# Kernel tuning notes

Hardware: AMD Instinct MI355X
Metric: run time of the kernel (lower is better)

## Reference

```python
import jax, jax.numpy as jnp
import numpy as np

B, H, S, D = 4, 8, 4096, 64

def setup_inputs() -> dict:
    key = jax.random.key(0)
    kq, kk, kv = jax.random.split(key, 3)
    Q = jax.random.normal(kq, (B, H, S, D), dtype=jnp.float32)
    K = jax.random.normal(kk, (B, H, S, D), dtype=jnp.float32)
    V = jax.random.normal(kv, (B, H, S, D), dtype=jnp.float32)
    return {"Q": Q, "K": K, "V": V}

def reference(Q, K, V):
    scale = 1.0 / jnp.sqrt(jnp.float32(Q.shape[-1]))
    # scores: [B, H, S, S]
    scores = jnp.einsum('bhqd,bhkd->bhqk', Q, K) * scale
    attn = jax.nn.softmax(scores, axis=-1)
    # out: [B, H, S, D]
    return jnp.einsum('bhqk,bhkd->bhqd', attn, V)
```

## Files before the change

kernel.cpp:

```cpp
#include <hip/hip_runtime.h>
#include <hip/hip_bf16.h>

typedef float  f32x16 __attribute__((ext_vector_type(16)));
typedef __bf16 bf16x8 __attribute__((ext_vector_type(8)));
typedef __bf16 bf16x4 __attribute__((ext_vector_type(4)));
typedef __bf16 bf16x2 __attribute__((ext_vector_type(2)));
typedef int    i32x2v __attribute__((ext_vector_type(2)));
typedef int    i32x4v __attribute__((ext_vector_type(4)));

#define SEQ   4096
#define DDIM  64
#define KB    64
#define NT    (SEQ / KB)
#define TILEB 16384
#define WSNEED (32ull * NT * TILEB)
#define SCL   0.18033688011112042f
#define DEFT  16.0f

#if __has_builtin(__builtin_amdgcn_exp2f)
#define EXP2(x) __builtin_amdgcn_exp2f(x)
#else
#define EXP2(x) __expf((x) * 0.6931471805599453f)
#endif

__device__ __forceinline__ int swzb(int row) {
  return (row & 7) ^ ((row >> 3) & 3);
}

__device__ __forceinline__ void pswap32(int &x, int &y) {
#if __has_builtin(__builtin_amdgcn_permlane32_swap)
  i32x2v r = __builtin_amdgcn_permlane32_swap(x, y, false, false);
  x = r[0]; y = r[1];
#else
  asm volatile("v_permlane32_swap_b32 %0, %1" : "+v"(x), "+v"(y));
#endif
}

__device__ __forceinline__ bf16x8 mkfrag(int a, int b, int c, int d) {
  i32x4v v; v[0] = a; v[1] = b; v[2] = c; v[3] = d;
  return __builtin_bit_cast(bf16x8, v);
}

__device__ __forceinline__ float max8(const f32x16& s, int o) {
  float m = fmaxf(fmaxf(s[o+0], s[o+1]), s[o+2]);
  m = fmaxf(fmaxf(m, s[o+3]), s[o+4]);
  m = fmaxf(fmaxf(m, s[o+5]), s[o+6]);
  return fmaxf(m, s[o+7]);
}

__global__ __launch_bounds__(256)
void prep(const float* __restrict__ Kg, const float* __restrict__ Vg,
          char* __restrict__ KVb)
{
  int i = blockIdx.x * 256 + threadIdx.x;
  if (i < (1 << 20)) {
    int row = i >> 3, s_in = i & 7;
    int bh = row >> 12, r = row & 4095, t = r >> 6, kv = r & 63;
    const float* src = Kg + (size_t)row * 64 + s_in * 8;
    float4 f0 = *(const float4*)(src);
    float4 f1 = *(const float4*)(src + 4);
    bf16x8 p;
    p[0] = (__bf16)f0.x; p[1] = (__bf16)f0.y; p[2] = (__bf16)f0.z; p[3] = (__bf16)f0.w;
    p[4] = (__bf16)f1.x; p[5] = (__bf16)f1.y; p[6] = (__bf16)f1.z; p[7] = (__bf16)f1.w;
    char* dst = KVb + (size_t)(bh * NT + t) * TILEB + kv * 128 + ((s_in ^ swzb(kv)) * 16);
    *(bf16x8*)dst = p;
  } else {
    int j = i - (1 << 20);
    int d = j & 63, rest = j >> 6;
    int kvg = rest & 7, t = (rest >> 3) & 63, bh = rest >> 9;
    const float* src = Vg + (size_t)bh * (SEQ * DDIM) + (t * 64 + kvg * 8) * 64 + d;
    bf16x8 p;
    #pragma unroll
    for (int jj = 0; jj < 8; ++jj) p[jj] = (__bf16)src[jj * 64];
    char* dst = KVb + (size_t)(bh * NT + t) * TILEB + 8192 + d * 128
              + ((kvg ^ swzb(d)) * 16);
    *(bf16x8*)dst = p;
  }
}

__global__ __launch_bounds__(256, 4)
void fattn(const float* __restrict__ Qg, const char* __restrict__ KVb,
           float* __restrict__ Og)
{
  __shared__ __align__(16) char smem[2 * TILEB];

  const int tid  = threadIdx.x;
  const int w    = tid >> 6;
  const int lane = tid & 63;
  const int q31  = lane & 31;
  const int h    = lane >> 5;

  int wg = (int)blockIdx.x;
  wg = (wg & 7) * 128 + (wg >> 3);
  const int bh = wg >> 5;
  const int qb = wg & 31;
  const size_t base = (size_t)bh * (SEQ * DDIM);
  const int qrow = qb * 128 + w * 32 + q31;

  bf16x8 aq[4];
  {
    const float* qp = Qg + base + (size_t)qrow * DDIM + 8 * h;
    #pragma unroll
    for (int c = 0; c < 4; ++c) {
      float4 f0 = *(const float4*)(qp + 16 * c);
      float4 f1 = *(const float4*)(qp + 16 * c + 4);
      aq[c][0] = (__bf16)(f0.x * SCL);
      aq[c][1] = (__bf16)(f0.y * SCL);
      aq[c][2] = (__bf16)(f0.z * SCL);
      aq[c][3] = (__bf16)(f0.w * SCL);
      aq[c][4] = (__bf16)(f1.x * SCL);
      aq[c][5] = (__bf16)(f1.y * SCL);
      aq[c][6] = (__bf16)(f1.z * SCL);
      aq[c][7] = (__bf16)(f1.w * SCL);
    }
  }

  const char* kvt = KVb + (size_t)bh * (NT * TILEB);
  const int soff = tid * 16;

  const int swr = swzb(q31) << 4;
  int kaddr[4];
  #pragma unroll
  for (int c = 0; c < 4; ++c)
    kaddr[c] = q31 * 128 + ((32 * c + 16 * h) ^ swr);

  f32x16 o0 = {}, o1 = {};
  float mrow = 0.f, lsum = 0.f;
  int pk[2][8];

  auto softmax_pack = [&](f32x16& s0, f32x16& s1) {
    float m0 = max8(s0, 0), m1 = max8(s0, 8);
    float m2 = max8(s1, 0), m3 = max8(s1, 8);
    float pm = fmaxf(fmaxf(m0, m1), fmaxf(m2, m3));
    if (!__all(pm <= mrow + DEFT)) {
      float tm = fmaxf(pm, __shfl_xor(pm, 32));
      float mn = fmaxf(mrow, tm);
      float corr = EXP2(mrow - mn);
      o0 *= corr; o1 *= corr; lsum *= corr;
      mrow = mn;
    }
    #pragma unroll
    for (int r = 0; r < 16; ++r) s0[r] = EXP2(s0[r] - mrow);
    #pragma unroll
    for (int r = 0; r < 16; ++r) s1[r] = EXP2(s1[r] - mrow);
    f32x16 ts = s0 + s1;
    lsum += ((((ts[0]+ts[1])+(ts[2]+ts[3])) + ((ts[4]+ts[5])+(ts[6]+ts[7])))
          +  (((ts[8]+ts[9])+(ts[10]+ts[11])) + ((ts[12]+ts[13])+(ts[14]+ts[15]))));
    #pragma unroll
    for (int u = 0; u < 8; ++u) {
      bf16x2 p0; p0[0] = (__bf16)s0[2*u]; p0[1] = (__bf16)s0[2*u+1];
      pk[0][u] = __builtin_bit_cast(int, p0);
      bf16x2 p1; p1[0] = (__bf16)s1[2*u]; p1[1] = (__bf16)s1[2*u+1];
      pk[1][u] = __builtin_bit_cast(int, p1);
    }
    #pragma unroll
    for (int m = 0; m < 2; ++m) {
      pswap32(pk[m][0], pk[m][2]);
      pswap32(pk[m][1], pk[m][3]);
      pswap32(pk[m][4], pk[m][6]);
      pswap32(pk[m][5], pk[m][7]);
    }
  };

  {
    const char* sp = kvt + soff;
    #pragma unroll
    for (int c = 0; c < 4; ++c)
      *(bf16x8*)(smem + soff + c * 4096) = *(const bf16x8*)(sp + c * 4096);
  }
  __syncthreads();

  for (int t = 0; t < NT; ++t) {
    const int cur  = (t & 1) << 14;
    const int nxtb = cur ^ TILEB;
    const bool more = (t + 1) < NT;

    bf16x8 st0, st1, st2, st3;
    if (more) {
      const char* sp = kvt + (size_t)(t + 1) * TILEB + soff;
      st0 = *(const bf16x8*)(sp);
      st1 = *(const bf16x8*)(sp + 4096);
      st2 = *(const bf16x8*)(sp + 8192);
      st3 = *(const bf16x8*)(sp + 12288);
    }

    f32x16 s0 = {}, s1 = {};
    __builtin_amdgcn_s_setprio(1);
    #pragma unroll
    for (int c = 0; c < 4; ++c) {
      bf16x8 k0 = *(const bf16x8*)(smem + cur + kaddr[c]);
      bf16x8 k1 = *(const bf16x8*)(smem + cur + kaddr[c] + 4096);
      s0 = __builtin_amdgcn_mfma_f32_32x32x16_bf16(k0, aq[c], s0, 0, 0, 0);
      s1 = __builtin_amdgcn_mfma_f32_32x32x16_bf16(k1, aq[c], s1, 0, 0, 0);
    }
    __builtin_amdgcn_s_setprio(0);

    if (more) {
      *(bf16x8*)(smem + nxtb + soff)        = st0;
      *(bf16x8*)(smem + nxtb + soff + 4096) = st1;
    }

    softmax_pack(s0, s1);

    __builtin_amdgcn_s_setprio(1);
    #pragma unroll
    for (int c = 0; c < 4; ++c) {
      bf16x8 bp = mkfrag(pk[c>>1][(c&1)*4+0], pk[c>>1][(c&1)*4+1],
                         pk[c>>1][(c&1)*4+2], pk[c>>1][(c&1)*4+3]);
      bf16x8 v0 = *(const bf16x8*)(smem + cur + kaddr[c] + 8192);
      bf16x8 v1 = *(const bf16x8*)(smem + cur + kaddr[c] + 12288);
      o0 = __builtin_amdgcn_mfma_f32_32x32x16_bf16(v0, bp, o0, 0, 0, 0);
      o1 = __builtin_amdgcn_mfma_f32_32x32x16_bf16(v1, bp, o1, 0, 0, 0);
    }
    __builtin_amdgcn_s_setprio(0);

    if (more) {
      *(bf16x8*)(smem + nxtb + soff + 8192)  = st2;
      *(bf16x8*)(smem + nxtb + soff + 12288) = st3;
    }
    __syncthreads();
  }

  float l = lsum + __shfl_xor(lsum, 32);
  float inv = 1.0f / l;
  float* op = Og + base + (size_t)qrow * DDIM + 4 * h;
  #pragma unroll
  for (int rg = 0; rg < 4; ++rg) {
    float4 st0 = { o0[4*rg+0]*inv, o0[4*rg+1]*inv, o0[4*rg+2]*inv, o0[4*rg+3]*inv };
    *(float4*)(op + 8*rg) = st0;
    float4 st1 = { o1[4*rg+0]*inv, o1[4*rg+1]*inv, o1[4*rg+2]*inv, o1[4*rg+3]*inv };
    *(float4*)(op + 8*rg + 32) = st1;
  }
}

__global__ __launch_bounds__(512)
void fattn_fb(const float* __restrict__ Qg, const float* __restrict__ Kg,
              const float* __restrict__ Vg, float* __restrict__ Og)
{
  __shared__ __align__(16) char smem[32768];
  const int tid  = threadIdx.x;
  const int w    = tid >> 6;
  const int lane = tid & 63;
  const int q31  = lane & 31;
  const int h    = lane >> 5;

  int wg = (int)blockIdx.x;
  wg = (wg & 7) * 64 + (wg >> 3);
  const int bh = wg >> 4;
  const int qb = wg & 15;
  const size_t base = (size_t)bh * (SEQ * DDIM);
  const int qrow = qb * 256 + w * 32 + q31;

  bf16x8 aq[4];
  {
    const float* qp = Qg + base + (size_t)qrow * DDIM + 8 * h;
    #pragma unroll
    for (int c = 0; c < 4; ++c) {
      float4 f0 = *(const float4*)(qp + 16 * c);
      float4 f1 = *(const float4*)(qp + 16 * c + 4);
      aq[c][0] = (__bf16)(f0.x * SCL); aq[c][1] = (__bf16)(f0.y * SCL);
      aq[c][2] = (__bf16)(f0.z * SCL); aq[c][3] = (__bf16)(f0.w * SCL);
      aq[c][4] = (__bf16)(f1.x * SCL); aq[c][5] = (__bf16)(f1.y * SCL);
      aq[c][6] = (__bf16)(f1.z * SCL); aq[c][7] = (__bf16)(f1.w * SCL);
    }
  }

  const int kvA = tid >> 4;
  const int dK  = (tid & 15) * 4;
  const int kw0 = ((kvA * 128 + dK * 2) ^ (swzb(kvA) << 4));
  const int kv0 = (tid >> 4) * 2;
  const int dV  = (tid & 15) * 4;
  int vw[4];
  #pragma unroll
  for (int qq = 0; qq < 4; ++qq)
    vw[qq] = 8192 + (((dV + qq) * 128 + kv0 * 2) ^ (swzb(dV + qq) << 4));
  const float* kptr = Kg + base + (size_t)kvA * DDIM + dK;
  const float* vptr = Vg + base + (size_t)kv0 * DDIM + dV;

  const int swr = swzb(q31) << 4;
  int kaddr[4];
  #pragma unroll
  for (int c = 0; c < 4; ++c)
    kaddr[c] = q31 * 128 + ((32 * c + 16 * h) ^ swr);

  f32x16 o0 = {}, o1 = {};
  float mrow = 0.f, lsum = 0.f;

  {
    float4 ka = *(const float4*)(kptr);
    float4 kb = *(const float4*)(kptr + 32 * DDIM);
    float4 va = *(const float4*)(vptr);
    float4 vb = *(const float4*)(vptr + DDIM);
    bf16x4 pa, pb;
    pa[0]=(__bf16)ka.x; pa[1]=(__bf16)ka.y; pa[2]=(__bf16)ka.z; pa[3]=(__bf16)ka.w;
    pb[0]=(__bf16)kb.x; pb[1]=(__bf16)kb.y; pb[2]=(__bf16)kb.z; pb[3]=(__bf16)kb.w;
    *(bf16x4*)(smem + kw0)            = pa;
    *(bf16x4*)(smem + kw0 + 32 * 128) = pb;
    float va4[4] = {va.x, va.y, va.z, va.w};
    float vb4[4] = {vb.x, vb.y, vb.z, vb.w};
    #pragma unroll
    for (int qq = 0; qq < 4; ++qq) {
      bf16x2 p; p[0] = (__bf16)va4[qq]; p[1] = (__bf16)vb4[qq];
      *(bf16x2*)(smem + vw[qq]) = p;
    }
  }

  int rbase = 0;
  for (int t = 0; t < NT; ++t) {
    __syncthreads();
    const bool more = (t + 1) < NT;
    const float* kpt = kptr + (size_t)(t + 1) * (KB * DDIM);
    const float* vpt = vptr + (size_t)(t + 1) * (KB * DDIM);
    float4 ka = {}, kb = {};
    if (more) { ka = *(const float4*)(kpt); kb = *(const float4*)(kpt + 32 * DDIM); }

    f32x16 s0 = {}, s1 = {};
    #pragma unroll
    for (int c = 0; c < 4; ++c) {
      bf16x8 k0 = *(const bf16x8*)(smem + rbase + kaddr[c]);
      bf16x8 k1 = *(const bf16x8*)(smem + rbase + kaddr[c] + 4096);
      s0 = __builtin_amdgcn_mfma_f32_32x32x16_bf16(k0, aq[c], s0, 0, 0, 0);
      s1 = __builtin_amdgcn_mfma_f32_32x32x16_bf16(k1, aq[c], s1, 0, 0, 0);
    }

    float4 va = {}, vb = {};
    if (more) { va = *(const float4*)(vpt); vb = *(const float4*)(vpt + DDIM); }

    float pm;
    {
      float m0 = max8(s0, 0), m1 = max8(s0, 8);
      float m2 = max8(s1, 0), m3 = max8(s1, 8);
      pm = fmaxf(fmaxf(m0, m1), fmaxf(m2, m3));
    }
    if (!__all(pm <= mrow + DEFT)) {
      float tm = fmaxf(pm, __shfl_xor(pm, 32));
      float mn = fmaxf(mrow, tm);
      float corr = EXP2(mrow - mn);
      o0 *= corr; o1 *= corr; lsum *= corr;
      mrow = mn;
    }
    #pragma unroll
    for (int r = 0; r < 16; ++r) s0[r] = EXP2(s0[r] - mrow);
    #pragma unroll
    for (int r = 0; r < 16; ++r) s1[r] = EXP2(s1[r] - mrow);
    f32x16 ts = s0 + s1;
    lsum += ((((ts[0]+ts[1])+(ts[2]+ts[3])) + ((ts[4]+ts[5])+(ts[6]+ts[7])))
          +  (((ts[8]+ts[9])+(ts[10]+ts[11])) + ((ts[12]+ts[13])+(ts[14]+ts[15]))));

    int pk[2][8];
    #pragma unroll
    for (int u = 0; u < 8; ++u) {
      bf16x2 p0; p0[0] = (__bf16)s0[2*u]; p0[1] = (__bf16)s0[2*u+1];
      pk[0][u] = __builtin_bit_cast(int, p0);
      bf16x2 p1; p1[0] = (__bf16)s1[2*u]; p1[1] = (__bf16)s1[2*u+1];
      pk[1][u] = __builtin_bit_cast(int, p1);
    }
    #pragma unroll
    for (int m = 0; m < 2; ++m) {
      pswap32(pk[m][0], pk[m][2]); pswap32(pk[m][1], pk[m][3]);
      pswap32(pk[m][4], pk[m][6]); pswap32(pk[m][5], pk[m][7]);
    }

    const int wb = rbase ^ 16384;
    if (more) {
      bf16x4 pa, pb;
      pa[0]=(__bf16)ka.x; pa[1]=(__bf16)ka.y; pa[2]=(__bf16)ka.z; pa[3]=(__bf16)ka.w;
      pb[0]=(__bf16)kb.x; pb[1]=(__bf16)kb.y; pb[2]=(__bf16)kb.z; pb[3]=(__bf16)kb.w;
      *(bf16x4*)(smem + wb + kw0)            = pa;
      *(bf16x4*)(smem + wb + kw0 + 32 * 128) = pb;
    }

    #pragma unroll
    for (int c = 0; c < 4; ++c) {
      bf16x8 bp = mkfrag(pk[c>>1][(c&1)*4+0], pk[c>>1][(c&1)*4+1],
                         pk[c>>1][(c&1)*4+2], pk[c>>1][(c&1)*4+3]);
      bf16x8 v0 = *(const bf16x8*)(smem + rbase + kaddr[c] + 8192);
      bf16x8 v1 = *(const bf16x8*)(smem + rbase + kaddr[c] + 12288);
      o0 = __builtin_amdgcn_mfma_f32_32x32x16_bf16(v0, bp, o0, 0, 0, 0);
      o1 = __builtin_amdgcn_mfma_f32_32x32x16_bf16(v1, bp, o1, 0, 0, 0);
    }

    if (more) {
      float va4[4] = {va.x, va.y, va.z, va.w};
      float vb4[4] = {vb.x, vb.y, vb.z, vb.w};
      #pragma unroll
      for (int qq = 0; qq < 4; ++qq) {
        bf16x2 p; p[0] = (__bf16)va4[qq]; p[1] = (__bf16)vb4[qq];
        *(bf16x2*)(smem + wb + vw[qq]) = p;
      }
    }
    rbase ^= 16384;
  }

  float l = lsum + __shfl_xor(lsum, 32);
  float inv = 1.0f / l;
  float* op = Og + base + (size_t)qrow * DDIM + 4 * h;
  #pragma unroll
  for (int rg = 0; rg < 4; ++rg) {
    float4 w0 = { o0[4*rg+0]*inv, o0[4*rg+1]*inv, o0[4*rg+2]*inv, o0[4*rg+3]*inv };
    *(float4*)(op + 8*rg) = w0;
    float4 w1 = { o1[4*rg+0]*inv, o1[4*rg+1]*inv, o1[4*rg+2]*inv, o1[4*rg+3]*inv };
    *(float4*)(op + 8*rg + 32) = w1;
  }
}

extern "C" void kernel_launch(void* const* d_in, const int* in_sizes, int n_in,
                              void* d_out, int out_size, void* d_ws, size_t ws_size,
                              hipStream_t stream) {
  const float* Q = (const float*)d_in[0];
  const float* K = (const float*)d_in[1];
  const float* V = (const float*)d_in[2];
  float* O = (float*)d_out;
  if (ws_size >= WSNEED) {
    prep<<<dim3(8192), dim3(256), 0, stream>>>(K, V, (char*)d_ws);
    fattn<<<dim3(1024), dim3(256), 0, stream>>>(Q, (const char*)d_ws, O);
  } else {
    fattn_fb<<<dim3(512), dim3(512), 0, stream>>>(Q, K, V, O);
  }
}
```

Before: 191.3 us.

## Stream K/V tiles directly into LDS and skip max subtraction before first rescale

Replaces the register-staged prefetch of the next K/V tile (global load into VGPRs, then ds_write) with global_load_lds direct-to-LDS transfers issued at the top of each iteration. This frees the staging registers and removes the explicit LDS store instructions, letting the copy overlap with the MFMA work. It also adds a flag so that, until the running max first moves off zero, the exponentials skip the subtraction of the row max. The risks are correctness of the async LDS writes relative to the barrier and waitcnt handling, plus an extra per-wave branch in the softmax.

Result: no change. 192.7 us (+0.7%).

```diff
diff --git a/kernel.cpp b/kernel.cpp
--- a/kernel.cpp
+++ b/kernel.cpp
@@ -34,6 +34,12 @@
 #else
   asm volatile("v_permlane32_swap_b32 %0, %1" : "+v"(x), "+v"(y));
 #endif
+}
+
+__device__ __forceinline__ void gl_lds16(const char* g, char* l) {
+  __builtin_amdgcn_global_load_lds(
+      (const __attribute__((address_space(1))) void*)g,
+      (__attribute__((address_space(3))) void*)l, 16, 0, 0);
 }
 
 __device__ __forceinline__ bf16x8 mkfrag(int a, int b, int c, int d) {
@@ -116,7 +122,8 @@
   }
 
   const char* kvt = KVb + (size_t)bh * (NT * TILEB);
-  const int soff = tid * 16;
+  const int stg   = w * 1024 + lane * 16;
+  const int ldsw  = w * 1024;
 
   const int swr = swzb(q31) << 4;
   int kaddr[4];
@@ -126,6 +133,7 @@
 
   f32x16 o0 = {}, o1 = {};
   float mrow = 0.f, lsum = 0.f;
+  int mzero = 1;
   int pk[2][8];
 
   auto softmax_pack = [&](f32x16& s0, f32x16& s1) {
@@ -137,12 +145,19 @@
       float mn = fmaxf(mrow, tm);
       float corr = EXP2(mrow - mn);
       o0 *= corr; o1 *= corr; lsum *= corr;
-      mrow = mn;
-    }
-    #pragma unroll
-    for (int r = 0; r < 16; ++r) s0[r] = EXP2(s0[r] - mrow);
-    #pragma unroll
-    for (int r = 0; r < 16; ++r) s1[r] = EXP2(s1[r] - mrow);
+      mrow = mn; mzero = 0;
+    }
+    if (__builtin_expect(mzero, 1)) {
+      #pragma unroll
+      for (int r = 0; r < 16; ++r) s0[r] = EXP2(s0[r]);
+      #pragma unroll
+      for (int r = 0; r < 16; ++r) s1[r] = EXP2(s1[r]);
+    } else {
+      #pragma unroll
+      for (int r = 0; r < 16; ++r) s0[r] = EXP2(s0[r] - mrow);
+      #pragma unroll
+      for (int r = 0; r < 16; ++r) s1[r] = EXP2(s1[r] - mrow);
+    }
     f32x16 ts = s0 + s1;
     lsum += ((((ts[0]+ts[1])+(ts[2]+ts[3])) + ((ts[4]+ts[5])+(ts[6]+ts[7])))
           +  (((ts[8]+ts[9])+(ts[10]+ts[11])) + ((ts[12]+ts[13])+(ts[14]+ts[15]))));
@@ -163,10 +178,10 @@
   };
 
   {
-    const char* sp = kvt + soff;
+    const char* gp = kvt + stg;
     #pragma unroll
     for (int c = 0; c < 4; ++c)
-      *(bf16x8*)(smem + soff + c * 4096) = *(const bf16x8*)(sp + c * 4096);
+      gl_lds16(gp + c * 4096, smem + ldsw + c * 4096);
   }
   __syncthreads();
 
@@ -175,13 +190,11 @@
     const int nxtb = cur ^ TILEB;
     const bool more = (t + 1) < NT;
 
-    bf16x8 st0, st1, st2, st3;
     if (more) {
-      const char* sp = kvt + (size_t)(t + 1) * TILEB + soff;
-      st0 = *(const bf16x8*)(sp);
-      st1 = *(const bf16x8*)(sp + 4096);
-      st2 = *(const bf16x8*)(sp + 8192);
-      st3 = *(const bf16x8*)(sp + 12288);
+      const char* gp = kvt + (size_t)(t + 1) * TILEB + stg;
+      #pragma unroll
+      for (int c = 0; c < 4; ++c)
+        gl_lds16(gp + c * 4096, smem + nxtb + ldsw + c * 4096);
     }
 
     f32x16 s0 = {}, s1 = {};
@@ -194,11 +207,6 @@
       s1 = __builtin_amdgcn_mfma_f32_32x32x16_bf16(k1, aq[c], s1, 0, 0, 0);
     }
     __builtin_amdgcn_s_setprio(0);
-
-    if (more) {
-      *(bf16x8*)(smem + nxtb + soff)        = st0;
-      *(bf16x8*)(smem + nxtb + soff + 4096) = st1;
-    }
 
     softmax_pack(s0, s1);
 
@@ -214,10 +222,6 @@
     }
     __builtin_amdgcn_s_setprio(0);
 
-    if (more) {
-      *(bf16x8*)(smem + nxtb + soff + 8192)  = st2;
-      *(bf16x8*)(smem + nxtb + soff + 12288) = st3;
-    }
     __syncthreads();
   }
 
```
